# Performance work log

Hardware: AMD Instinct MI355X
Metric: run time of the kernel (lower is better)

The kernel has to match this reference:

```python
import jax, jax.numpy as jnp
import numpy as np

T, IN, M, C, OUT = 8192, 1024, 64, 16, 1024  # time, input, trace, context, output


def _ln(x, eps=1e-5):
    mu = jnp.mean(x, axis=-1, keepdims=True)
    var = jnp.var(x, axis=-1, keepdims=True)
    return (x - mu) * jax.lax.rsqrt(var + eps)


def _mish(x):
    return x * jnp.tanh(jax.nn.softplus(x))


def setup_inputs() -> dict:
    key = jax.random.key(0)
    ks = jax.random.split(key, 8)

    def w(k, o, i):
        return (jax.random.normal(k, (o, i), jnp.float32) / np.sqrt(i).astype(np.float32))

    return {
        "x": jax.random.normal(ks[0], (T, IN), jnp.float32),
        "state0": jnp.zeros((1, M, C), jnp.float32),  # real part of complex zero init
        "start": jax.random.uniform(ks[1], (T,)) < 0.002,  # sparse episode resets
        "next_done": jnp.zeros((T,), bool),  # unused by the sequential-equivalent math
        "a": jnp.linspace(1e-6, 0.5, M, dtype=jnp.float32),  # ffa.init decay
        "bf": (2.0 * jnp.pi / jnp.linspace(1.0, 1024.0, C)).astype(jnp.float32),  # ffa.init freqs
        "pre_w": w(ks[2], M, IN), "pre_b": jnp.zeros((M,), jnp.float32),
        "skip_w": w(ks[3], OUT, IN), "skip_b": jnp.zeros((OUT,), jnp.float32),
        "mix_w1": w(ks[4], M * C, 2 * M * C), "mix_b1": jnp.zeros((M * C,), jnp.float32),
        "mix_w2": w(ks[5], M * C, M * C), "mix_b2": jnp.zeros((M * C,), jnp.float32),
        "mix_w3": w(ks[6], OUT, M * C), "mix_b3": jnp.zeros((OUT,), jnp.float32),
    }


def _forward(x, state0, start, a, bf, pre_w, pre_b, skip_w, skip_b,
             mix_w1, mix_b1, mix_w2, mix_b2, mix_w3, mix_b3):
    Tn = x.shape[0]
    # pre = softplus(Linear(LayerNorm(x)))  -> [T, M]
    pre = jax.nn.softplus(_ln(x) @ pre_w.T + pre_b)
    # one-step FFA decay gamma[m,c] = exp(-|a_m| + i*b_c)
    la = jnp.broadcast_to(-jnp.abs(a)[:, None], (a.shape[0], bf.shape[0]))
    lb = jnp.broadcast_to(bf[None, :], la.shape)
    gamma = jnp.exp(jax.lax.complex(la, lb))  # [M, C] complex64
    # reset monoid: s_t = A_t * s_{t-1} + b_t,  A_t = 0 where episode starts
    A = jnp.where(start[:, None, None], jnp.zeros((), gamma.dtype), gamma[None])  # [T,M,C]
    b_el = jnp.broadcast_to(pre[:, :, None].astype(gamma.dtype), A.shape)  # [T,M,C]
    s_init = state0.astype(gamma.dtype)  # [1, M, C]
    b_el = b_el.at[0].add(A[0] * s_init[0])  # fold carried state into first element

    def combine(lhs, rhs):
        Al, bl = lhs
        Ar, br = rhs
        return Ar * Al, Ar * bl + br

    _, s = jax.lax.associative_scan(combine, (A, b_el))  # s: [T, M, C] states at every t

    s_flat = s.reshape(Tn, M * C)
    # global (all-element) complex mean / real std normalization, as in the source
    scaled = (s_flat - jnp.mean(s_flat)) / (1e-6 + jnp.std(s_flat))
    z = jnp.concatenate([scaled.real, scaled.imag], axis=-1)  # [T, 2*M*C]
    z = _mish(z @ mix_w1.T + mix_b1)
    z = _mish(z @ mix_w2.T + mix_b2)
    z = z @ mix_w3.T + mix_b3  # [T, OUT]
    out = _ln(z + (x @ skip_w.T + skip_b))
    return out, s[-1:]


def reference(x, state0, start, next_done, a, bf, pre_w, pre_b, skip_w, skip_b,
              mix_w1, mix_b1, mix_w2, mix_b2, mix_w3, mix_b3):
    return _forward(x, state0, start, a, bf, pre_w, pre_b, skip_w, skip_b,
                    mix_w1, mix_b1, mix_w2, mix_b2, mix_w3, mix_b3)
```

## Files before the change

### kernel.cpp

```cpp
#include <hip/hip_runtime.h>
#include <hip/hip_bf16.h>

#define T_    8192
#define INDIM 1024
#define MTR   64
#define CCTX  16
#define MC    1024
#define NOUT  1024
#define CHUNK 64
#define NCH   128

using bf16x8 = __attribute__((ext_vector_type(8))) short;
using f32x4  = __attribute__((ext_vector_type(4))) float;

__device__ __forceinline__ unsigned short f2bf(float f) {
  unsigned int u = __builtin_bit_cast(unsigned int, f);
  u += 0x7fffu + ((u >> 16) & 1u);
  return (unsigned short)(u >> 16);
}

__device__ __forceinline__ float mish_f(float v) {
  float u = __expf(v);
  float w = u * (u + 2.f);
  return (v > 20.f) ? v : v * __fdividef(w, w + 2.f);
}

typedef __attribute__((address_space(1))) void gas_void;
typedef __attribute__((address_space(3))) void las_void;

__device__ __forceinline__ void gload_lds16(const void* g, void* l) {
  __builtin_amdgcn_global_load_lds((gas_void*)g, (las_void*)l, 16, 0, 0);
}

__global__ __launch_bounds__(256) void cast4_k(const float* __restrict__ w1, const float* __restrict__ w2,
                                               const float* __restrict__ w3, const float* __restrict__ sw,
                                               unsigned short* __restrict__ o1, unsigned short* __restrict__ o2,
                                               unsigned short* __restrict__ o3, unsigned short* __restrict__ o4) {
  long i = ((long)blockIdx.x * 256 + threadIdx.x) * 4;
  const float* src; unsigned short* dst; long off;
  if (i < 2097152)      { src = w1; dst = o1; off = i; }
  else if (i < 3145728) { src = w2; dst = o2; off = i - 2097152; }
  else if (i < 4194304) { src = w3; dst = o3; off = i - 3145728; }
  else if (i < 5242880) { src = sw; dst = o4; off = i - 4194304; }
  else return;
  float4 v = *(const float4*)(src + off);
  ushort4 o = { f2bf(v.x), f2bf(v.y), f2bf(v.z), f2bf(v.w) };
  *(ushort4*)(dst + off) = o;
}

__device__ __forceinline__ float2 block_sum2(float s, float ss, float* sbuf) {
#pragma unroll
  for (int off = 32; off > 0; off >>= 1) {
    s  += __shfl_down(s, off);
    ss += __shfl_down(ss, off);
  }
  if ((threadIdx.x & 63) == 0) {
    sbuf[(threadIdx.x >> 6) * 2]     = s;
    sbuf[(threadIdx.x >> 6) * 2 + 1] = ss;
  }
  __syncthreads();
  return make_float2(sbuf[0] + sbuf[2] + sbuf[4] + sbuf[6],
                     sbuf[1] + sbuf[3] + sbuf[5] + sbuf[7]);
}

__global__ __launch_bounds__(256) void ln_cast_k(const float* __restrict__ x,
                                                 float2* __restrict__ rowstat,
                                                 unsigned short* __restrict__ xb) {
  __shared__ float sbuf[8];
  const long row = blockIdx.x;
  float4 v = ((const float4*)(x + (row << 10)))[threadIdx.x];
  ushort4 c = { f2bf(v.x), f2bf(v.y), f2bf(v.z), f2bf(v.w) };
  ((ushort4*)(xb + (row << 10)))[threadIdx.x] = c;
  float2 t = block_sum2(v.x + v.y + v.z + v.w,
                        v.x * v.x + v.y * v.y + v.z * v.z + v.w * v.w, sbuf);
  float mean = t.x * (1.f / 1024.f);
  float var  = t.y * (1.f / 1024.f) - mean * mean;
  float rstd = rsqrtf(var + 1e-5f);
  if (threadIdx.x == 0) rowstat[row] = make_float2(mean, rstd);
}

__global__ __launch_bounds__(256) void ln_out1_k(const float* __restrict__ p, float* __restrict__ out) {
  __shared__ float sbuf[8];
  const long row = blockIdx.x;
  float4 v = ((const float4*)(p + (row << 10)))[threadIdx.x];
  float2 t = block_sum2(v.x + v.y + v.z + v.w,
                        v.x * v.x + v.y * v.y + v.z * v.z + v.w * v.w, sbuf);
  float mean = t.x * (1.f / 1024.f);
  float var  = t.y * (1.f / 1024.f) - mean * mean;
  float rstd = rsqrtf(var + 1e-5f);
  float4 o = { (v.x - mean) * rstd, (v.y - mean) * rstd,
               (v.z - mean) * rstd, (v.w - mean) * rstd };
  ((float4*)(out + (row << 10)))[threadIdx.x] = o;
}

__global__ __launch_bounds__(256) void pre_part_k(const float* __restrict__ x,
                                                  const float2* __restrict__ rowstat,
                                                  const float* __restrict__ pw,
                                                  float* __restrict__ part) {
  const int lane = threadIdx.x & 63;
  const int wvu  = __builtin_amdgcn_readfirstlane(threadIdx.x >> 6);
  const int kc   = blockIdx.y;
  const int r0   = (blockIdx.x * 4 + wvu) * 32;

  const float* wrow = pw + (long)lane * 1024 + kc * 128;
  float wreg[128];
#pragma unroll
  for (int j = 0; j < 32; ++j)
    *(float4*)&wreg[j * 4] = ((const float4*)wrow)[j];
  float swsum = 0.f;
#pragma unroll
  for (int j = 0; j < 128; ++j) swsum += wreg[j];

  float* po = part + ((long)kc * T_ + r0) * 64 + lane;
  const float* xbase = x + (long)r0 * 1024 + kc * 128;

  for (int i = 0; i < 32; i += 2) {
    const float4* xr0 = (const float4*)(xbase + (long)i * 1024);
    const float4* xr1 = (const float4*)(xbase + (long)(i + 1) * 1024);
    float a0 = 0.f, a1 = 0.f, a2 = 0.f, a3 = 0.f;
    float b0 = 0.f, b1 = 0.f, b2 = 0.f, b3 = 0.f;
#pragma unroll
    for (int j = 0; j < 32; j += 4) {
      float4 xa0 = xr0[j],     xa1 = xr0[j + 1], xa2 = xr0[j + 2], xa3 = xr0[j + 3];
      float4 xb0 = xr1[j],     xb1 = xr1[j + 1], xb2 = xr1[j + 2], xb3 = xr1[j + 3];
      a0 += wreg[4*j+0]*xa0.x  + wreg[4*j+1]*xa0.y  + wreg[4*j+2]*xa0.z  + wreg[4*j+3]*xa0.w;
      a1 += wreg[4*j+4]*xa1.x  + wreg[4*j+5]*xa1.y  + wreg[4*j+6]*xa1.z  + wreg[4*j+7]*xa1.w;
      a2 += wreg[4*j+8]*xa2.x  + wreg[4*j+9]*xa2.y  + wreg[4*j+10]*xa2.z + wreg[4*j+11]*xa2.w;
      a3 += wreg[4*j+12]*xa3.x + wreg[4*j+13]*xa3.y + wreg[4*j+14]*xa3.z + wreg[4*j+15]*xa3.w;
      b0 += wreg[4*j+0]*xb0.x  + wreg[4*j+1]*xb0.y  + wreg[4*j+2]*xb0.z  + wreg[4*j+3]*xb0.w;
      b1 += wreg[4*j+4]*xb1.x  + wreg[4*j+5]*xb1.y  + wreg[4*j+6]*xb1.z  + wreg[4*j+7]*xb1.w;
      b2 += wreg[4*j+8]*xb2.x  + wreg[4*j+9]*xb2.y  + wreg[4*j+10]*xb2.z + wreg[4*j+11]*xb2.w;
      b3 += wreg[4*j+12]*xb3.x + wreg[4*j+13]*xb3.y + wreg[4*j+14]*xb3.z + wreg[4*j+15]*xb3.w;
    }
    float2 s0 = rowstat[r0 + i];
    float2 s1 = rowstat[r0 + i + 1];
    po[(long)i * 64]       = s0.y * ((a0 + a1) + (a2 + a3)) - s0.x * s0.y * swsum;
    po[(long)(i + 1) * 64] = s1.y * ((b0 + b1) + (b2 + b3)) - s1.x * s1.y * swsum;
  }
}

__global__ __launch_bounds__(256) void pre_fin_k(const float* __restrict__ part,
                                                 const float* __restrict__ pb,
                                                 float* __restrict__ pre) {
  long i = (long)blockIdx.x * 256 + threadIdx.x;
  int m = (int)(i & 63);
  float s = 0.f;
#pragma unroll
  for (int kc = 0; kc < 8; ++kc)
    s += part[(long)kc * T_ * 64 + i];
  float v = s + pb[m];
  float sp = fmaxf(v, 0.f) + log1pf(expf(-fabsf(v)));
  pre[i] = sp;
}

__global__ __launch_bounds__(256) void scan_p1(const float* __restrict__ pre, const int* __restrict__ start,
                                               const float* __restrict__ a, const float* __restrict__ bfr,
                                               double2* __restrict__ chA, double2* __restrict__ chB) {
  int ch = blockIdx.y * 256 + threadIdx.x;
  int m = ch >> 4, c = ch & 15;
  double dec = exp(-fabs((double)a[m]));
  double th = (double)bfr[c];
  double gre = dec * cos(th), gim = dec * sin(th);
  int j = blockIdx.x;
  int t0 = j * CHUNK;
  double pr = 1.0, pi = 0.0, sr = 0.0, si = 0.0;
  for (int t = t0; t < t0 + CHUNK; ++t) {
    double b = (double)pre[(long)t * 64 + m];
    if (start[t]) {
      pr = 0.0; pi = 0.0; sr = b; si = 0.0;
    } else {
      double nsr = gre * sr - gim * si + b;
      si = gre * si + gim * sr; sr = nsr;
      double npr = gre * pr - gim * pi;
      pi = gre * pi + gim * pr; pr = npr;
    }
  }
  chA[j * MC + ch] = make_double2(pr, pi);
  chB[j * MC + ch] = make_double2(sr, si);
}

__global__ __launch_bounds__(256) void scan_p2(const double2* __restrict__ chA, const double2* __restrict__ chB,
                                               const float* __restrict__ state0,
                                               double2* __restrict__ carry, double* __restrict__ red,
                                               float* __restrict__ out_tail, int fmt) {
  if (blockIdx.x == 0 && threadIdx.x < 4) red[threadIdx.x] = 0.0;
  int ch = blockIdx.x * 256 + threadIdx.x;
  double cr = (double)state0[ch], ci = 0.0;
  for (int j = 0; j < NCH; ++j) {
    carry[j * MC + ch] = make_double2(cr, ci);
    double2 A = chA[j * MC + ch];
    double2 B = chB[j * MC + ch];
    double ncr = A.x * cr - A.y * ci + B.x;
    ci = A.x * ci + A.y * cr + B.y;
    cr = ncr;
  }
  if (fmt == 1024) {
    out_tail[ch] = (float)cr;
  } else {
    out_tail[2 * ch]     = (float)cr;
    out_tail[2 * ch + 1] = (float)ci;
  }
}

__global__ __launch_bounds__(256) void scan_p3(const float* __restrict__ pre, const int* __restrict__ start,
                                               const float* __restrict__ a, const float* __restrict__ bfr,
                                               const double2* __restrict__ carry,
                                               double* __restrict__ red) {
  __shared__ double sbuf[12];
  int ch = blockIdx.y * 256 + threadIdx.x;
  int m = ch >> 4, c = ch & 15;
  double dec = exp(-fabs((double)a[m]));
  double th = (double)bfr[c];
  double gre = dec * cos(th), gim = dec * sin(th);
  int j = blockIdx.x;
  int t0 = j * CHUNK;
  double2 cin = carry[j * MC + ch];
  double sr = cin.x, si = cin.y;
  double aR = 0.0, aI = 0.0, aS = 0.0;
  for (int t = t0; t < t0 + CHUNK; ++t) {
    double b = (double)pre[(long)t * 64 + m];
    if (start[t]) { sr = b; si = 0.0; }
    else {
      double nsr = gre * sr - gim * si + b;
      si = gre * si + gim * sr; sr = nsr;
    }
    aR += sr; aI += si; aS += sr * sr + si * si;
  }
#pragma unroll
  for (int off = 32; off > 0; off >>= 1) {
    aR += __shfl_down(aR, off); aI += __shfl_down(aI, off); aS += __shfl_down(aS, off);
  }
  if ((threadIdx.x & 63) == 0) {
    int w = threadIdx.x >> 6;
    sbuf[w * 3] = aR; sbuf[w * 3 + 1] = aI; sbuf[w * 3 + 2] = aS;
  }
  __syncthreads();
  if (threadIdx.x == 0) {
    atomicAdd(&red[0], sbuf[0] + sbuf[3] + sbuf[6] + sbuf[9]);
    atomicAdd(&red[1], sbuf[1] + sbuf[4] + sbuf[7] + sbuf[10]);
    atomicAdd(&red[2], sbuf[2] + sbuf[5] + sbuf[8] + sbuf[11]);
  }
}

__global__ void finalize_red(const double* __restrict__ red, float* __restrict__ redf) {
  const double n = (double)T_ * (double)MC;
  double mre = red[0] / n, mim = red[1] / n;
  double var = red[2] / n - mre * mre - mim * mim;
  double sd = sqrt(var > 0.0 ? var : 0.0);
  redf[0] = (float)mre;
  redf[1] = (float)mim;
  redf[2] = (float)(1.0 / (1e-6 + sd));
}

__global__ __launch_bounds__(256) void zscan_k(const float* __restrict__ pre, const int* __restrict__ start,
                                               const float* __restrict__ a, const float* __restrict__ bfr,
                                               const double2* __restrict__ carry, const float* __restrict__ redf,
                                               unsigned short* __restrict__ z) {
  int ch = blockIdx.y * 256 + threadIdx.x;
  int m = ch >> 4, c = ch & 15;
  double dec = exp(-fabs((double)a[m]));
  double th = (double)bfr[c];
  double gre = dec * cos(th), gim = dec * sin(th);
  int j = blockIdx.x;
  int t0 = j * CHUNK;
  double2 cin = carry[j * MC + ch];
  double sr = cin.x, si = cin.y;
  const float mre = redf[0], mim = redf[1], inv = redf[2];
  for (int t = t0; t < t0 + CHUNK; ++t) {
    double b = (double)pre[(long)t * 64 + m];
    if (start[t]) { sr = b; si = 0.0; }
    else {
      double nsr = gre * sr - gim * si + b;
      si = gre * si + gim * sr; sr = nsr;
    }
    z[(long)t * 2048 + ch]        = f2bf(((float)sr - mre) * inv);
    z[(long)t * 2048 + 1024 + ch] = f2bf(((float)si - mim) * inv);
  }
}

template<int EP>
__global__ __launch_bounds__(256) void gemm_bt(const unsigned short* __restrict__ A,
                                               const unsigned short* __restrict__ B,
                                               const float* __restrict__ bias,
                                               const float* __restrict__ add,
                                               void* __restrict__ Cout,
                                               int M_, int N_, int K_) {
  __shared__ __align__(16) unsigned short lA[2][128 * 32];
  __shared__ __align__(16) unsigned short lB[2][128 * 32];
  const int tid = threadIdx.x;
  const int lane = tid & 63;
  const int wv = tid >> 6;
  const int wr = wv >> 1, wc = wv & 1;
  const long brow = (long)blockIdx.x * 128;
  const long bcol = (long)blockIdx.y * 128;

  f32x4 acc[4][4];
#pragma unroll
  for (int i = 0; i < 4; i++)
#pragma unroll
    for (int j = 0; j < 4; j++)
      acc[i][j] = f32x4{0.f, 0.f, 0.f, 0.f};

  const int c0 = tid, c1 = tid + 256;
  const long ar0 = brow + (c0 >> 2), ar1 = brow + (c1 >> 2);
  const long br0 = bcol + (c0 >> 2), br1 = bcol + (c1 >> 2);
  const int ko0 = (((c0 & 3) ^ ((c0 >> 3) & 3)) * 8);
  const int ko1 = (((c1 & 3) ^ ((c1 >> 3) & 3)) * 8);
  const int r15 = lane & 15;
  const int swzq = (((lane >> 4) ^ ((r15 >> 1) & 3)) * 8);

  gload_lds16(A + ar0 * K_ + ko0, &lA[0][c0 * 8]);
  gload_lds16(A + ar1 * K_ + ko1, &lA[0][c1 * 8]);
  gload_lds16(B + br0 * K_ + ko0, &lB[0][c0 * 8]);
  gload_lds16(B + br1 * K_ + ko1, &lB[0][c1 * 8]);

  int cur = 0;
  for (int kt = 0; kt < K_; kt += 32) {
    const int nxt = cur ^ 1;
    if (kt + 32 < K_) {
      gload_lds16(A + ar0 * K_ + (kt + 32) + ko0, &lA[nxt][c0 * 8]);
      gload_lds16(A + ar1 * K_ + (kt + 32) + ko1, &lA[nxt][c1 * 8]);
      gload_lds16(B + br0 * K_ + (kt + 32) + ko0, &lB[nxt][c0 * 8]);
      gload_lds16(B + br1 * K_ + (kt + 32) + ko1, &lB[nxt][c1 * 8]);
      asm volatile("s_waitcnt vmcnt(4)" ::: "memory");
    } else {
      asm volatile("s_waitcnt vmcnt(0)" ::: "memory");
    }
    __builtin_amdgcn_sched_barrier(0);
    __builtin_amdgcn_s_barrier();
    __builtin_amdgcn_sched_barrier(0);

    bf16x8 af[4], bv[4];
#pragma unroll
    for (int mi = 0; mi < 4; mi++)
      af[mi] = *(const bf16x8*)&lA[cur][(wr * 64 + mi * 16 + r15) * 32 + swzq];
#pragma unroll
    for (int nj = 0; nj < 4; nj++)
      bv[nj] = *(const bf16x8*)&lB[cur][(wc * 64 + nj * 16 + r15) * 32 + swzq];
#pragma unroll
    for (int mi = 0; mi < 4; mi++)
#pragma unroll
      for (int nj = 0; nj < 4; nj++)
        acc[mi][nj] = __builtin_amdgcn_mfma_f32_16x16x32_bf16(af[mi], bv[nj], acc[mi][nj], 0, 0, 0);

    __builtin_amdgcn_sched_barrier(0);
    __builtin_amdgcn_s_barrier();
    cur = nxt;
  }

  const int rq = (lane >> 4) * 4;
#pragma unroll
  for (int nj = 0; nj < 4; nj++) {
    const long col = bcol + wc * 64 + nj * 16 + r15;
    const float bs = bias[col];
#pragma unroll
    for (int mi = 0; mi < 4; mi++) {
#pragma unroll
      for (int r = 0; r < 4; r++) {
        const long row = brow + wr * 64 + mi * 16 + rq + r;
        float v = acc[mi][nj][r] + bs;
        if (EP == 0) {
          ((float*)Cout)[row * N_ + col] = v;
        } else if (EP == 3) {
          ((float*)Cout)[row * N_ + col] = v + add[row * N_ + col];
        } else {
          ((unsigned short*)Cout)[row * N_ + col] = f2bf(mish_f(v));
        }
      }
    }
  }
}

extern "C" void kernel_launch(void* const* d_in, const int* in_sizes, int n_in,
                              void* d_out, int out_size, void* d_ws, size_t ws_size,
                              hipStream_t stream) {
  (void)in_sizes; (void)n_in; (void)ws_size;
  const float* x      = (const float*)d_in[0];
  const float* state0 = (const float*)d_in[1];
  const int*   start  = (const int*)d_in[2];
  const float* a      = (const float*)d_in[4];
  const float* bfr    = (const float*)d_in[5];
  const float* pre_w  = (const float*)d_in[6];
  const float* pre_b  = (const float*)d_in[7];
  const float* skip_w = (const float*)d_in[8];
  const float* skip_b = (const float*)d_in[9];
  const float* w1     = (const float*)d_in[10];
  const float* b1     = (const float*)d_in[11];
  const float* w2     = (const float*)d_in[12];
  const float* b2     = (const float*)d_in[13];
  const float* w3     = (const float*)d_in[14];
  const float* b3     = (const float*)d_in[15];

  char* ws = (char*)d_ws;
  const size_t MB = 1u << 20;
  float*          skipf = (float*)(ws + 0);
  float*          part  = (float*)(ws + 32 * MB);
  float*          h3    = (float*)(ws + 32 * MB);
  unsigned short* z     = (unsigned short*)(ws + 64 * MB);
  unsigned short* xb    = (unsigned short*)(ws + 96 * MB);
  unsigned short* h2    = (unsigned short*)(ws + 96 * MB);
  unsigned short* h1    = (unsigned short*)(ws + 112 * MB);
  unsigned short* wb1   = (unsigned short*)(ws + 128 * MB);
  unsigned short* wb2   = (unsigned short*)(ws + 132 * MB);
  unsigned short* wb3   = (unsigned short*)(ws + 134 * MB);
  unsigned short* skwb  = (unsigned short*)(ws + 136 * MB);
  float*          pre   = (float*)(ws + 138 * MB);
  double2*        chA   = (double2*)(ws + 140 * MB);
  double2*        chB   = (double2*)(ws + 142 * MB);
  double2*        carry = (double2*)(ws + 144 * MB);
  double*         red   = (double*)(ws + 146 * MB);
  float*          redf  = (float*)(ws + 146 * MB + 64);
  float2*         rowst = (float2*)(ws + 147 * MB);

  cast4_k<<<5120, 256, 0, stream>>>(w1, w2, w3, skip_w, wb1, wb2, wb3, skwb);

  ln_cast_k<<<8192, 256, 0, stream>>>(x, rowst, xb);
  pre_part_k<<<dim3(64, 8), 256, 0, stream>>>(x, rowst, pre_w, part);
  pre_fin_k<<<2048, 256, 0, stream>>>(part, pre_b, pre);

  int tail_elems = out_size - T_ * NOUT;
  float* out_tail = (float*)d_out + (long)T_ * NOUT;
  scan_p1<<<dim3(NCH, 4), 256, 0, stream>>>(pre, start, a, bfr, chA, chB);
  scan_p2<<<4, 256, 0, stream>>>(chA, chB, state0, carry, red, out_tail, tail_elems);
  scan_p3<<<dim3(NCH, 4), 256, 0, stream>>>(pre, start, a, bfr, carry, red);
  finalize_red<<<1, 1, 0, stream>>>(red, redf);

  zscan_k<<<dim3(NCH, 4), 256, 0, stream>>>(pre, start, a, bfr, carry, redf, z);

  gemm_bt<0><<<dim3(64, 8), 256, 0, stream>>>(xb, skwb, skip_b, nullptr, skipf, T_, 1024, 1024);
  gemm_bt<2><<<dim3(64, 8), 256, 0, stream>>>(z,  wb1, b1, nullptr, h1, T_, 1024, 2048);
  gemm_bt<2><<<dim3(64, 8), 256, 0, stream>>>(h1, wb2, b2, nullptr, h2, T_, 1024, 1024);
  gemm_bt<3><<<dim3(64, 8), 256, 0, stream>>>(h2, wb3, b3, skipf, h3, T_, 1024, 1024);

  ln_out1_k<<<8192, 256, 0, stream>>>(h3, (float*)d_out);
}
```

Measured before the change: 307.8 us.

## Use 64x128 GEMM tiles, fuse skip and first MLP GEMMs into one launch

The GEMM kernel moves from 128x128 to 64x128 tiles with four waves each owning a 32-column slice, doubling the block count from 512 to 1024 per GEMM so the many CUs are better filled. The skip GEMM and the first mix GEMM run in a single dual launch of 2048 blocks, so the two independent GEMMs execute concurrently and the skip GEMM no longer needs its own launch. scan_p2 is split into 16 blocks of 64 threads to spread the serial carry pass over more CUs. Smaller tiles lower data reuse per block and raise operand reloads from global memory.

```diff
diff --git a/kernel.cpp b/kernel.cpp
--- a/kernel.cpp
+++ b/kernel.cpp
@@ -179,12 +179,12 @@
   chB[j * MC + ch] = make_double2(sr, si);
 }
 
-__global__ __launch_bounds__(256) void scan_p2(const double2* __restrict__ chA, const double2* __restrict__ chB,
-                                               const float* __restrict__ state0,
-                                               double2* __restrict__ carry, double* __restrict__ red,
-                                               float* __restrict__ out_tail, int fmt) {
+__global__ __launch_bounds__(64) void scan_p2(const double2* __restrict__ chA, const double2* __restrict__ chB,
+                                              const float* __restrict__ state0,
+                                              double2* __restrict__ carry, double* __restrict__ red,
+                                              float* __restrict__ out_tail, int fmt) {
   if (blockIdx.x == 0 && threadIdx.x < 4) red[threadIdx.x] = 0.0;
-  int ch = blockIdx.x * 256 + threadIdx.x;
+  int ch = blockIdx.x * 64 + threadIdx.x;
   double cr = (double)state0[ch], ci = 0.0;
   for (int j = 0; j < NCH; ++j) {
     carry[j * MC + ch] = make_double2(cr, ci);
@@ -278,51 +278,50 @@
   }
 }
 
+#define LA_SZ (64 * 32)
+#define LB_SZ (128 * 32)
 template<int EP>
-__global__ __launch_bounds__(256) void gemm_bt(const unsigned short* __restrict__ A,
-                                               const unsigned short* __restrict__ B,
-                                               const float* __restrict__ bias,
-                                               const float* __restrict__ add,
-                                               void* __restrict__ Cout,
-                                               int M_, int N_, int K_) {
-  __shared__ __align__(16) unsigned short lA[2][128 * 32];
-  __shared__ __align__(16) unsigned short lB[2][128 * 32];
+__device__ __forceinline__ void gemm64_core(const unsigned short* __restrict__ A,
+                                            const unsigned short* __restrict__ B,
+                                            const float* __restrict__ bias,
+                                            const float* __restrict__ add,
+                                            void* __restrict__ Cout,
+                                            int bx, int by, int N_, int K_,
+                                            unsigned short* lA, unsigned short* lB) {
   const int tid = threadIdx.x;
   const int lane = tid & 63;
   const int wv = tid >> 6;
-  const int wr = wv >> 1, wc = wv & 1;
-  const long brow = (long)blockIdx.x * 128;
-  const long bcol = (long)blockIdx.y * 128;
-
-  f32x4 acc[4][4];
+  const long brow = (long)bx * 64;
+  const long bcol = (long)by * 128;
+
+  f32x4 acc[4][2];
 #pragma unroll
   for (int i = 0; i < 4; i++)
 #pragma unroll
-    for (int j = 0; j < 4; j++)
+    for (int j = 0; j < 2; j++)
       acc[i][j] = f32x4{0.f, 0.f, 0.f, 0.f};
 
-  const int c0 = tid, c1 = tid + 256;
-  const long ar0 = brow + (c0 >> 2), ar1 = brow + (c1 >> 2);
-  const long br0 = bcol + (c0 >> 2), br1 = bcol + (c1 >> 2);
-  const int ko0 = (((c0 & 3) ^ ((c0 >> 3) & 3)) * 8);
-  const int ko1 = (((c1 & 3) ^ ((c1 >> 3) & 3)) * 8);
+  const int c0 = tid, cb1 = tid + 256;
+  const long ar0 = brow + (c0 >> 2);
+  const long br0 = bcol + (c0 >> 2);
+  const long br1 = bcol + (cb1 >> 2);
+  const int koA  = (((c0 & 3) ^ ((c0 >> 3) & 3)) * 8);
+  const int koB1 = (((cb1 & 3) ^ ((cb1 >> 3) & 3)) * 8);
   const int r15 = lane & 15;
   const int swzq = (((lane >> 4) ^ ((r15 >> 1) & 3)) * 8);
 
-  gload_lds16(A + ar0 * K_ + ko0, &lA[0][c0 * 8]);
-  gload_lds16(A + ar1 * K_ + ko1, &lA[0][c1 * 8]);
-  gload_lds16(B + br0 * K_ + ko0, &lB[0][c0 * 8]);
-  gload_lds16(B + br1 * K_ + ko1, &lB[0][c1 * 8]);
+  gload_lds16(A + ar0 * K_ + koA,  lA + c0 * 8);
+  gload_lds16(B + br0 * K_ + koA,  lB + c0 * 8);
+  gload_lds16(B + br1 * K_ + koB1, lB + cb1 * 8);
 
   int cur = 0;
   for (int kt = 0; kt < K_; kt += 32) {
     const int nxt = cur ^ 1;
     if (kt + 32 < K_) {
-      gload_lds16(A + ar0 * K_ + (kt + 32) + ko0, &lA[nxt][c0 * 8]);
-      gload_lds16(A + ar1 * K_ + (kt + 32) + ko1, &lA[nxt][c1 * 8]);
-      gload_lds16(B + br0 * K_ + (kt + 32) + ko0, &lB[nxt][c0 * 8]);
-      gload_lds16(B + br1 * K_ + (kt + 32) + ko1, &lB[nxt][c1 * 8]);
-      asm volatile("s_waitcnt vmcnt(4)" ::: "memory");
+      gload_lds16(A + ar0 * K_ + (kt + 32) + koA,  lA + nxt * LA_SZ + c0 * 8);
+      gload_lds16(B + br0 * K_ + (kt + 32) + koA,  lB + nxt * LB_SZ + c0 * 8);
+      gload_lds16(B + br1 * K_ + (kt + 32) + koB1, lB + nxt * LB_SZ + cb1 * 8);
+      asm volatile("s_waitcnt vmcnt(3)" ::: "memory");
     } else {
       asm volatile("s_waitcnt vmcnt(0)" ::: "memory");
     }
@@ -330,17 +329,17 @@
     __builtin_amdgcn_s_barrier();
     __builtin_amdgcn_sched_barrier(0);
 
-    bf16x8 af[4], bv[4];
+    bf16x8 af[4], bv[2];
 #pragma unroll
     for (int mi = 0; mi < 4; mi++)
-      af[mi] = *(const bf16x8*)&lA[cur][(wr * 64 + mi * 16 + r15) * 32 + swzq];
-#pragma unroll
-    for (int nj = 0; nj < 4; nj++)
-      bv[nj] = *(const bf16x8*)&lB[cur][(wc * 64 + nj * 16 + r15) * 32 + swzq];
+      af[mi] = *(const bf16x8*)&lA[cur * LA_SZ + (mi * 16 + r15) * 32 + swzq];
+#pragma unroll
+    for (int nj = 0; nj < 2; nj++)
+      bv[nj] = *(const bf16x8*)&lB[cur * LB_SZ + (wv * 32 + nj * 16 + r15) * 32 + swzq];
 #pragma unroll
     for (int mi = 0; mi < 4; mi++)
 #pragma unroll
-      for (int nj = 0; nj < 4; nj++)
+      for (int nj = 0; nj < 2; nj++)
         acc[mi][nj] = __builtin_amdgcn_mfma_f32_16x16x32_bf16(af[mi], bv[nj], acc[mi][nj], 0, 0, 0);
 
     __builtin_amdgcn_sched_barrier(0);
@@ -350,14 +349,14 @@
 
   const int rq = (lane >> 4) * 4;
 #pragma unroll
-  for (int nj = 0; nj < 4; nj++) {
-    const long col = bcol + wc * 64 + nj * 16 + r15;
+  for (int nj = 0; nj < 2; nj++) {
+    const long col = bcol + wv * 32 + nj * 16 + r15;
     const float bs = bias[col];
 #pragma unroll
     for (int mi = 0; mi < 4; mi++) {
 #pragma unroll
       for (int r = 0; r < 4; r++) {
-        const long row = brow + wr * 64 + mi * 16 + rq + r;
+        const long row = brow + mi * 16 + rq + r;
         float v = acc[mi][nj][r] + bs;
         if (EP == 0) {
           ((float*)Cout)[row * N_ + col] = v;
@@ -368,6 +367,36 @@
         }
       }
     }
+  }
+}
+
+template<int EP>
+__global__ __launch_bounds__(256) void gemm64_k(const unsigned short* __restrict__ A,
+                                                const unsigned short* __restrict__ B,
+                                                const float* __restrict__ bias,
+                                                const float* __restrict__ add,
+                                                void* __restrict__ Cout, int N_, int K_) {
+  __shared__ __align__(16) unsigned short lA[2 * LA_SZ];
+  __shared__ __align__(16) unsigned short lB[2 * LB_SZ];
+  gemm64_core<EP>(A, B, bias, add, Cout, blockIdx.x, blockIdx.y, N_, K_, lA, lB);
+}
+
+__global__ __launch_bounds__(256) void gemm_dual(const unsigned short* __restrict__ A1,
+                                                 const unsigned short* __restrict__ B1,
+                                                 const float* __restrict__ bias1,
+                                                 unsigned short* __restrict__ C1, int K1,
+                                                 const unsigned short* __restrict__ A2,
+                                                 const unsigned short* __restrict__ B2,
+                                                 const float* __restrict__ bias2,
+                                                 float* __restrict__ C2, int K2) {
+  __shared__ __align__(16) unsigned short lA[2 * LA_SZ];
+  __shared__ __align__(16) unsigned short lB[2 * LB_SZ];
+  int b = blockIdx.x;
+  if (b < 1024) {
+    gemm64_core<2>(A1, B1, bias1, nullptr, C1, b & 127, b >> 7, 1024, K1, lA, lB);
+  } else {
+    b -= 1024;
+    gemm64_core<0>(A2, B2, bias2, nullptr, C2, b & 127, b >> 7, 1024, K2, lA, lB);
   }
 }
 
@@ -421,16 +450,15 @@
   int tail_elems = out_size - T_ * NOUT;
   float* out_tail = (float*)d_out + (long)T_ * NOUT;
   scan_p1<<<dim3(NCH, 4), 256, 0, stream>>>(pre, start, a, bfr, chA, chB);
-  scan_p2<<<4, 256, 0, stream>>>(chA, chB, state0, carry, red, out_tail, tail_elems);
+  scan_p2<<<16, 64, 0, stream>>>(chA, chB, state0, carry, red, out_tail, tail_elems);
   scan_p3<<<dim3(NCH, 4), 256, 0, stream>>>(pre, start, a, bfr, carry, red);
   finalize_red<<<1, 1, 0, stream>>>(red, redf);
 
   zscan_k<<<dim3(NCH, 4), 256, 0, stream>>>(pre, start, a, bfr, carry, redf, z);
 
-  gemm_bt<0><<<dim3(64, 8), 256, 0, stream>>>(xb, skwb, skip_b, nullptr, skipf, T_, 1024, 1024);
-  gemm_bt<2><<<dim3(64, 8), 256, 0, stream>>>(z,  wb1, b1, nullptr, h1, T_, 1024, 2048);
-  gemm_bt<2><<<dim3(64, 8), 256, 0, stream>>>(h1, wb2, b2, nullptr, h2, T_, 1024, 1024);
-  gemm_bt<3><<<dim3(64, 8), 256, 0, stream>>>(h2, wb3, b3, skipf, h3, T_, 1024, 1024);
+  gemm_dual<<<2048, 256, 0, stream>>>(z, wb1, b1, h1, 2048, xb, skwb, skip_b, skipf, 1024);
+  gemm64_k<2><<<dim3(128, 8), 256, 0, stream>>>(h1, wb2, b2, nullptr, h2, 1024, 1024);
+  gemm64_k<3><<<dim3(128, 8), 256, 0, stream>>>(h2, wb3, b3, skipf, h3, 1024, 1024);
 
   ln_out1_k<<<8192, 256, 0, stream>>>(h3, (float*)d_out);
 }
```

Measured after the change: 331.9 us. 1.08x slower.

## Deepen GEMM LDS pipeline to four stages and co-launch skip with first MLP GEMM

Applied to the files above, without the earlier changes.

The GEMM main loop moves from a double-buffered LDS ring to a four-buffer ring that keeps three tiles of global-to-LDS loads in flight, with vmcnt waits adjusted to match. The skip-projection GEMM and the first MLP GEMM are merged into one 1024-block launch so the two independent GEMMs share the GPU and fill more CUs than 512 blocks would. scan_p2 is split into 16 blocks of 64 threads to spread its serial carry loop across more CUs. The cost is 64 KB of LDS per block, which can lower occupancy, and the merged launch takes on the resource use of the heavier branch.

```diff
diff --git a/kernel.cpp b/kernel.cpp
--- a/kernel.cpp
+++ b/kernel.cpp
@@ -179,12 +179,12 @@
   chB[j * MC + ch] = make_double2(sr, si);
 }
 
-__global__ __launch_bounds__(256) void scan_p2(const double2* __restrict__ chA, const double2* __restrict__ chB,
-                                               const float* __restrict__ state0,
-                                               double2* __restrict__ carry, double* __restrict__ red,
-                                               float* __restrict__ out_tail, int fmt) {
+__global__ __launch_bounds__(64) void scan_p2(const double2* __restrict__ chA, const double2* __restrict__ chB,
+                                              const float* __restrict__ state0,
+                                              double2* __restrict__ carry, double* __restrict__ red,
+                                              float* __restrict__ out_tail, int fmt) {
   if (blockIdx.x == 0 && threadIdx.x < 4) red[threadIdx.x] = 0.0;
-  int ch = blockIdx.x * 256 + threadIdx.x;
+  int ch = blockIdx.x * 64 + threadIdx.x;
   double cr = (double)state0[ch], ci = 0.0;
   for (int j = 0; j < NCH; ++j) {
     carry[j * MC + ch] = make_double2(cr, ci);
@@ -278,21 +278,21 @@
   }
 }
 
+#define TSZ (128 * 32)
 template<int EP>
-__global__ __launch_bounds__(256) void gemm_bt(const unsigned short* __restrict__ A,
-                                               const unsigned short* __restrict__ B,
-                                               const float* __restrict__ bias,
-                                               const float* __restrict__ add,
-                                               void* __restrict__ Cout,
-                                               int M_, int N_, int K_) {
-  __shared__ __align__(16) unsigned short lA[2][128 * 32];
-  __shared__ __align__(16) unsigned short lB[2][128 * 32];
+__device__ __forceinline__ void gemm128_core(const unsigned short* __restrict__ A,
+                                             const unsigned short* __restrict__ B,
+                                             const float* __restrict__ bias,
+                                             const float* __restrict__ add,
+                                             void* __restrict__ Cout,
+                                             int bx, int by, int N_, int K_,
+                                             unsigned short* lA, unsigned short* lB) {
   const int tid = threadIdx.x;
   const int lane = tid & 63;
   const int wv = tid >> 6;
   const int wr = wv >> 1, wc = wv & 1;
-  const long brow = (long)blockIdx.x * 128;
-  const long bcol = (long)blockIdx.y * 128;
+  const long brow = (long)bx * 128;
+  const long bcol = (long)by * 128;
 
   f32x4 acc[4][4];
 #pragma unroll
@@ -309,34 +309,43 @@
   const int r15 = lane & 15;
   const int swzq = (((lane >> 4) ^ ((r15 >> 1) & 3)) * 8);
 
-  gload_lds16(A + ar0 * K_ + ko0, &lA[0][c0 * 8]);
-  gload_lds16(A + ar1 * K_ + ko1, &lA[0][c1 * 8]);
-  gload_lds16(B + br0 * K_ + ko0, &lB[0][c0 * 8]);
-  gload_lds16(B + br1 * K_ + ko1, &lB[0][c1 * 8]);
-
-  int cur = 0;
-  for (int kt = 0; kt < K_; kt += 32) {
-    const int nxt = cur ^ 1;
-    if (kt + 32 < K_) {
-      gload_lds16(A + ar0 * K_ + (kt + 32) + ko0, &lA[nxt][c0 * 8]);
-      gload_lds16(A + ar1 * K_ + (kt + 32) + ko1, &lA[nxt][c1 * 8]);
-      gload_lds16(B + br0 * K_ + (kt + 32) + ko0, &lB[nxt][c0 * 8]);
-      gload_lds16(B + br1 * K_ + (kt + 32) + ko1, &lB[nxt][c1 * 8]);
-      asm volatile("s_waitcnt vmcnt(4)" ::: "memory");
+  const int nt = K_ >> 5;
+
+#define STAGE(ti, bu)                                                      \
+  do {                                                                     \
+    gload_lds16(A + ar0 * K_ + (ti) * 32 + ko0, lA + (bu) * TSZ + c0 * 8); \
+    gload_lds16(A + ar1 * K_ + (ti) * 32 + ko1, lA + (bu) * TSZ + c1 * 8); \
+    gload_lds16(B + br0 * K_ + (ti) * 32 + ko0, lB + (bu) * TSZ + c0 * 8); \
+    gload_lds16(B + br1 * K_ + (ti) * 32 + ko1, lB + (bu) * TSZ + c1 * 8); \
+  } while (0)
+
+  STAGE(0, 0);
+  STAGE(1, 1);
+  STAGE(2, 2);
+
+  for (int i = 0; i < nt; ++i) {
+    if (i + 3 < nt) {
+      STAGE(i + 3, (i + 3) & 3);
+      asm volatile("s_waitcnt vmcnt(12)" ::: "memory");
     } else {
-      asm volatile("s_waitcnt vmcnt(0)" ::: "memory");
+      int r = nt - 1 - i;
+      if (r == 2)      asm volatile("s_waitcnt vmcnt(8)" ::: "memory");
+      else if (r == 1) asm volatile("s_waitcnt vmcnt(4)" ::: "memory");
+      else             asm volatile("s_waitcnt vmcnt(0)" ::: "memory");
     }
     __builtin_amdgcn_sched_barrier(0);
     __builtin_amdgcn_s_barrier();
     __builtin_amdgcn_sched_barrier(0);
 
+    const unsigned short* bA = lA + (i & 3) * TSZ;
+    const unsigned short* bB = lB + (i & 3) * TSZ;
     bf16x8 af[4], bv[4];
 #pragma unroll
     for (int mi = 0; mi < 4; mi++)
-      af[mi] = *(const bf16x8*)&lA[cur][(wr * 64 + mi * 16 + r15) * 32 + swzq];
+      af[mi] = *(const bf16x8*)&bA[(wr * 64 + mi * 16 + r15) * 32 + swzq];
 #pragma unroll
     for (int nj = 0; nj < 4; nj++)
-      bv[nj] = *(const bf16x8*)&lB[cur][(wc * 64 + nj * 16 + r15) * 32 + swzq];
+      bv[nj] = *(const bf16x8*)&bB[(wc * 64 + nj * 16 + r15) * 32 + swzq];
 #pragma unroll
     for (int mi = 0; mi < 4; mi++)
 #pragma unroll
@@ -345,8 +354,8 @@
 
     __builtin_amdgcn_sched_barrier(0);
     __builtin_amdgcn_s_barrier();
-    cur = nxt;
-  }
+  }
+#undef STAGE
 
   const int rq = (lane >> 4) * 4;
 #pragma unroll
@@ -368,6 +377,36 @@
         }
       }
     }
+  }
+}
+
+template<int EP>
+__global__ __launch_bounds__(256) void gemm128_k(const unsigned short* __restrict__ A,
+                                                 const unsigned short* __restrict__ B,
+                                                 const float* __restrict__ bias,
+                                                 const float* __restrict__ add,
+                                                 void* __restrict__ Cout, int N_, int K_) {
+  __shared__ __align__(16) unsigned short lA[4 * TSZ];
+  __shared__ __align__(16) unsigned short lB[4 * TSZ];
+  gemm128_core<EP>(A, B, bias, add, Cout, blockIdx.x, blockIdx.y, N_, K_, lA, lB);
+}
+
+__global__ __launch_bounds__(256) void gemm_dual128(const unsigned short* __restrict__ A1,
+                                                    const unsigned short* __restrict__ B1,
+                                                    const float* __restrict__ bias1,
+                                                    unsigned short* __restrict__ C1, int K1,
+                                                    const unsigned short* __restrict__ A2,
+                                                    const unsigned short* __restrict__ B2,
+                                                    const float* __restrict__ bias2,
+                                                    float* __restrict__ C2, int K2) {
+  __shared__ __align__(16) unsigned short lA[4 * TSZ];
+  __shared__ __align__(16) unsigned short lB[4 * TSZ];
+  int b = blockIdx.x;
+  if (b < 512) {
+    gemm128_core<2>(A1, B1, bias1, nullptr, C1, b & 63, b >> 6, 1024, K1, lA, lB);
+  } else {
+    b -= 512;
+    gemm128_core<0>(A2, B2, bias2, nullptr, C2, b & 63, b >> 6, 1024, K2, lA, lB);
   }
 }
 
@@ -421,16 +460,15 @@
   int tail_elems = out_size - T_ * NOUT;
   float* out_tail = (float*)d_out + (long)T_ * NOUT;
   scan_p1<<<dim3(NCH, 4), 256, 0, stream>>>(pre, start, a, bfr, chA, chB);
-  scan_p2<<<4, 256, 0, stream>>>(chA, chB, state0, carry, red, out_tail, tail_elems);
+  scan_p2<<<16, 64, 0, stream>>>(chA, chB, state0, carry, red, out_tail, tail_elems);
   scan_p3<<<dim3(NCH, 4), 256, 0, stream>>>(pre, start, a, bfr, carry, red);
   finalize_red<<<1, 1, 0, stream>>>(red, redf);
 
   zscan_k<<<dim3(NCH, 4), 256, 0, stream>>>(pre, start, a, bfr, carry, redf, z);
 
-  gemm_bt<0><<<dim3(64, 8), 256, 0, stream>>>(xb, skwb, skip_b, nullptr, skipf, T_, 1024, 1024);
-  gemm_bt<2><<<dim3(64, 8), 256, 0, stream>>>(z,  wb1, b1, nullptr, h1, T_, 1024, 2048);
-  gemm_bt<2><<<dim3(64, 8), 256, 0, stream>>>(h1, wb2, b2, nullptr, h2, T_, 1024, 1024);
-  gemm_bt<3><<<dim3(64, 8), 256, 0, stream>>>(h2, wb3, b3, skipf, h3, T_, 1024, 1024);
+  gemm_dual128<<<1024, 256, 0, stream>>>(z, wb1, b1, h1, 2048, xb, skwb, skip_b, skipf, 1024);
+  gemm128_k<2><<<dim3(64, 8), 256, 0, stream>>>(h1, wb2, b2, nullptr, h2, 1024, 1024);
+  gemm128_k<3><<<dim3(64, 8), 256, 0, stream>>>(h2, wb3, b3, skipf, h3, 1024, 1024);
 
   ln_out1_k<<<8192, 256, 0, stream>>>(h3, (float*)d_out);
 }
```

New measurement: 302.5 us. Within noise of the previous version (-1.7%).
